# Kernel tuning notes

Measured on AMD Instinct MI355X. Metric: run time of the kernel, lower is better.

Reference implementation:

```python
import jax, jax.numpy as jnp
import numpy as np

B, S, D, H = 4, 2048, 1024, 16
DH = D // H  # head dim = 64


def setup_inputs() -> dict:
    key = jax.random.key(0)
    ks = jax.random.split(key, 7)
    q = jax.random.normal(ks[0], (B, S, D), dtype=jnp.float32)
    k = jax.random.normal(ks[1], (B, S, D), dtype=jnp.float32)
    v = jax.random.normal(ks[2], (B, S, D), dtype=jnp.float32)
    mask = jax.random.uniform(ks[3], (1, S, S), dtype=jnp.float32)
    sc = 1.0 / np.sqrt(D)
    Wq = jax.random.normal(ks[4], (D, D), dtype=jnp.float32) * sc
    Wk = jax.random.normal(ks[5], (D, D), dtype=jnp.float32) * sc
    Wv = jax.random.normal(ks[6], (D, D), dtype=jnp.float32) * sc
    return {"q": q, "k": k, "v": v, "mask": mask, "Wq": Wq, "Wk": Wk, "Wv": Wv}


def reference(q, k, v, mask, Wq, Wk, Wv):
    # Linear projections (no bias), then split hidden into H heads.
    # tf.concat(tf.split(x, H, axis=2), axis=0) == reshape to (B,S,H,DH);
    # the final split/concat restores channel order [head0, head1, ...],
    # i.e. a plain (B,S,H,DH)->(B,S,D) reshape.
    qh = (q @ Wq).reshape(B, S, H, DH)
    kh = (k @ Wk).reshape(B, S, H, DH)
    vh = (v @ Wv).reshape(B, S, H, DH)
    score = jnp.einsum("bqhd,bkhd->bhqk", qh, kh) / jnp.sqrt(
        jnp.asarray(DH, dtype=q.dtype))
    # multiplicative mask applied BEFORE softmax (broadcast (1,Sq,Sk))
    score = score * mask[:, None, :, :][0:1].squeeze(0) if False else score * mask  # mask (1,Sq,Sk) broadcasts over (B,H,Sq,Sk)
    attn = jax.nn.softmax(score, axis=-1)
    out = jnp.einsum("bhqk,bkhd->bqhd", attn, vh).reshape(B, S, D)
    return out
```

## Files before the change

### kernel.cpp

```cpp
#include <hip/hip_runtime.h>

#define B_  4
#define S_  2048
#define D_  1024
#define H_  16
#define DH_ 64

typedef __attribute__((ext_vector_type(8))) short bf16x8;
typedef __attribute__((ext_vector_type(4))) float f32x4;
typedef __attribute__((ext_vector_type(16))) float f32x16;
typedef __attribute__((ext_vector_type(4))) unsigned short u16x4;

__device__ __forceinline__ unsigned short f2bf(float f) {
  union { float f; unsigned int u; } x; x.f = f;
  unsigned int u = x.u;
  unsigned int r = (u + 0x7fffu + ((u >> 16) & 1u)) >> 16;
  return (unsigned short)r;
}

__device__ __forceinline__ int cvtpk(float lo, float hi) {
  unsigned r;
  asm("v_cvt_pk_bf16_f32 %0, %1, %2" : "=v"(r) : "v"(lo), "v"(hi));
  return (int)r;
}

__global__ __launch_bounds__(256) void wtrans_kernel(const float* __restrict__ W0,
                                                     const float* __restrict__ W1,
                                                     const float* __restrict__ W2,
                                                     unsigned short* __restrict__ Wt) {
  __shared__ float t[32][33];
  const int z = blockIdx.z;
  const float* W = (z == 0) ? W0 : ((z == 1) ? W1 : W2);
  unsigned short* O = Wt + (size_t)z * (D_ * D_);
  const int n0 = blockIdx.x * 32, k0 = blockIdx.y * 32;
  const int tx = threadIdx.x, ty = threadIdx.y;
#pragma unroll
  for (int i = 0; i < 4; i++) t[ty + i * 8][tx] = W[(size_t)(k0 + ty + i * 8) * D_ + n0 + tx];
  __syncthreads();
#pragma unroll
  for (int i = 0; i < 4; i++)
    O[(size_t)(n0 + ty + i * 8) * D_ + k0 + tx] = f2bf(t[tx][ty + i * 8]);
}

__global__ __launch_bounds__(256) void proj_kernel(const float* __restrict__ X0,
                                                   const float* __restrict__ X1,
                                                   const float* __restrict__ X2,
                                                   const unsigned short* __restrict__ Wt,
                                                   unsigned short* __restrict__ Y0) {
  __shared__ __align__(16) unsigned short smem[2 * 128 * 72];
  unsigned short* Alds = smem;
  unsigned short* Blds = smem + 128 * 72;
  const int z = blockIdx.z;
  const float* X = (z == 0) ? X0 : ((z == 1) ? X1 : X2);
  const unsigned short* Wz = Wt + (size_t)z * (D_ * D_);
  unsigned short* Y = Y0 + (size_t)z * ((size_t)B_ * S_ * D_);
  const float osc = (z == 0) ? 0.18033688f : 1.0f;

  const int tid = threadIdx.x;
  const int lane = tid & 63, w = tid >> 6;
  const int wr = w >> 1, wc = w & 1;
  const int l15 = lane & 15, lg = lane >> 4;
  const int r0 = blockIdx.y * 128, c0 = blockIdx.x * 128;

  f32x4 acc[4][4];
#pragma unroll
  for (int m = 0; m < 4; m++)
#pragma unroll
    for (int n = 0; n < 4; n++) acc[m][n] = (f32x4){0.f, 0.f, 0.f, 0.f};

  for (int kt = 0; kt < 16; ++kt) {
    __syncthreads();
    {
      const int rr = tid >> 4, cf = (tid & 15) * 4;
#pragma unroll
      for (int p = 0; p < 8; p++) {
        int row = rr + p * 16;
        float4 xv = *(const float4*)(X + (size_t)(r0 + row) * D_ + kt * 64 + cf);
        u16x4 bb = { f2bf(xv.x), f2bf(xv.y), f2bf(xv.z), f2bf(xv.w) };
        *(u16x4*)(&Alds[row * 72 + cf]) = bb;
      }
      const int rb = tid >> 3, cb = tid & 7;
#pragma unroll
      for (int p = 0; p < 4; p++) {
        int row = rb + p * 32;
        bf16x8 wv = *(const bf16x8*)(Wz + (size_t)(c0 + row) * D_ + kt * 64 + cb * 8);
        *(bf16x8*)(&Blds[row * 72 + cb * 8]) = wv;
      }
    }
    __syncthreads();

    bf16x8 af[4][2];
#pragma unroll
    for (int m = 0; m < 4; m++)
#pragma unroll
      for (int kc = 0; kc < 2; kc++)
        af[m][kc] = *(const bf16x8*)(&Alds[(wr * 64 + m * 16 + l15) * 72 + kc * 32 + lg * 8]);
#pragma unroll
    for (int n = 0; n < 4; n++) {
      bf16x8 bfr[2];
#pragma unroll
      for (int kc = 0; kc < 2; kc++)
        bfr[kc] = *(const bf16x8*)(&Blds[(wc * 64 + n * 16 + l15) * 72 + kc * 32 + lg * 8]);
#pragma unroll
      for (int m = 0; m < 4; m++)
#pragma unroll
        for (int kc = 0; kc < 2; kc++)
          acc[m][n] = __builtin_amdgcn_mfma_f32_16x16x32_bf16(af[m][kc], bfr[kc], acc[m][n], 0, 0, 0);
    }
  }

  if (z == 2) {
    __syncthreads();
#pragma unroll
    for (int m = 0; m < 4; m++)
#pragma unroll
      for (int n = 0; n < 4; n++)
#pragma unroll
        for (int r = 0; r < 4; r++) {
          int srow = wr * 64 + m * 16 + lg * 4 + r;
          int dcol = wc * 64 + n * 16 + l15;
          smem[dcol * 136 + srow] = f2bf(acc[m][n][r]);
        }
    __syncthreads();
    const int dl = tid >> 1, sh = (tid & 1) * 64;
    const int bb = r0 >> 11, s0 = r0 & 2047;
    const int hh = (c0 + dl) >> 6, dd = (c0 + dl) & 63;
    size_t gbase = ((size_t)(bb * H_ + hh) * DH_ + dd) * (size_t)S_ + s0 + sh;
#pragma unroll
    for (int j = 0; j < 8; j++)
      *(bf16x8*)(Y + gbase + j * 8) = *(const bf16x8*)(&smem[dl * 136 + sh + j * 8]);
  } else {
#pragma unroll
    for (int m = 0; m < 4; m++)
#pragma unroll
      for (int n = 0; n < 4; n++)
#pragma unroll
        for (int r = 0; r < 4; r++) {
          int row = r0 + wr * 64 + m * 16 + lg * 4 + r;
          int col = c0 + wc * 64 + n * 16 + l15;
          Y[(size_t)row * D_ + col] = f2bf(acc[m][n][r] * osc);
        }
  }
}

__global__ __launch_bounds__(256) void attn_kernel(
    const unsigned short* __restrict__ qh,
    const unsigned short* __restrict__ kh,
    const unsigned short* __restrict__ vt,
    const float* __restrict__ mask,
    float* __restrict__ out) {
  __shared__ __align__(16) unsigned short K_lds[2][64 * 72];
  __shared__ __align__(16) unsigned short V_lds[2][64 * 72];

  const int tid = threadIdx.x;
  const int lane = tid & 63, w = tid >> 6;
  const int l31 = lane & 31, hf = lane >> 5;
  const int q0 = blockIdx.x * 128;
  const int h = blockIdx.y, b = blockIdx.z;
  const size_t head = (size_t)b * S_ * D_ + h * DH_;
  const int qrow = q0 + w * 32 + l31;

  bf16x8 bq[4];
  {
    const unsigned short* qp = qh + head + (size_t)qrow * D_;
#pragma unroll
    for (int ds = 0; ds < 4; ds++) bq[ds] = *(const bf16x8*)(qp + ds * 16 + hf * 8);
  }

  const int rr = tid >> 3, cc = tid & 7;
  const unsigned short* kbase = kh + head + (size_t)rr * D_ + cc * 8;
  const unsigned short* vtb = vt + ((size_t)(b * H_ + h) * DH_ + rr) * (size_t)S_ + cc * 8;

  f32x16 o_acc[2];
#pragma unroll
  for (int dt = 0; dt < 2; dt++)
#pragma unroll
    for (int r = 0; r < 16; r++) o_acc[dt][r] = 0.f;
  float m_r = -INFINITY, l_r = 0.f;

  {
#pragma unroll
    for (int p = 0; p < 2; p++) {
      bf16x8 kreg = *(const bf16x8*)(kbase + (size_t)p * 32 * D_);
      bf16x8 vreg = *(const bf16x8*)(vtb + (size_t)p * 32 * S_);
      int row = rr + p * 32;
      *(bf16x8*)(&K_lds[0][row * 72 + cc * 8]) = kreg;
      int byt = (row * 144 + cc * 16) ^ (((row >> 3) & 7) << 4);
      *(bf16x8*)((char*)&V_lds[0][0] + byt) = vreg;
    }
    __syncthreads();
  }

  for (int kt = 0; kt < 32; kt++) {
    const int cur = kt & 1;
    const bool more = (kt + 1 < 32);

    const int ktn = more ? kt + 1 : kt;
    bf16x8 kreg2[2], vreg2[2];
#pragma unroll
    for (int p = 0; p < 2; p++) {
      kreg2[p] = *(const bf16x8*)(kbase + (size_t)ktn * 64 * D_ + (size_t)p * 32 * D_);
      vreg2[p] = *(const bf16x8*)(vtb + (size_t)ktn * 64 + (size_t)p * 32 * S_);
    }
    __builtin_amdgcn_sched_barrier(0);

    f32x16 sacc[2];
#pragma unroll
    for (int ct = 0; ct < 2; ct++)
#pragma unroll
      for (int r = 0; r < 16; r++) sacc[ct][r] = 0.f;
    __builtin_amdgcn_s_setprio(1);
#pragma unroll
    for (int ds = 0; ds < 4; ds++)
#pragma unroll
      for (int ct = 0; ct < 2; ct++) {
        bf16x8 ak = *(const bf16x8*)(&K_lds[cur][(ct * 32 + l31) * 72 + ds * 16 + hf * 8]);
        sacc[ct] = __builtin_amdgcn_mfma_f32_32x32x16_bf16(ak, bq[ds], sacc[ct], 0, 0, 0);
      }
    __builtin_amdgcn_s_setprio(0);

    const float* mrow = mask + (size_t)qrow * S_ + kt * 64 + hf * 4;
#pragma unroll
    for (int ct = 0; ct < 2; ct++)
#pragma unroll
      for (int rq = 0; rq < 4; rq++) {
        float4 mk = *(const float4*)(mrow + ct * 32 + rq * 8);
        sacc[ct][rq * 4 + 0] *= mk.x;
        sacc[ct][rq * 4 + 1] *= mk.y;
        sacc[ct][rq * 4 + 2] *= mk.z;
        sacc[ct][rq * 4 + 3] *= mk.w;
      }

    float red[16];
#pragma unroll
    for (int i = 0; i < 16; i++) red[i] = fmaxf(sacc[0][i], sacc[1][i]);
#pragma unroll
    for (int off = 8; off >= 1; off >>= 1)
#pragma unroll
      for (int i = 0; i < off; i++) red[i] = fmaxf(red[i], red[i + off]);
    float tm = fmaxf(red[0], __shfl_xor(red[0], 32));

    float mn;
    if (__any(tm > m_r + 8.0f)) {
      mn = fmaxf(m_r, tm);
      float alpha = exp2f(m_r - mn);
      m_r = mn;
      l_r *= alpha;
#pragma unroll
      for (int dt = 0; dt < 2; dt++)
#pragma unroll
        for (int r = 0; r < 16; r++) o_acc[dt][r] *= alpha;
    } else {
      mn = m_r;
    }

#pragma unroll
    for (int ct = 0; ct < 2; ct++)
#pragma unroll
      for (int r = 0; r < 16; r++) sacc[ct][r] = exp2f(sacc[ct][r] - mn);

    float sr[16];
#pragma unroll
    for (int i = 0; i < 16; i++) sr[i] = sacc[0][i] + sacc[1][i];
#pragma unroll
    for (int off = 8; off >= 1; off >>= 1)
#pragma unroll
      for (int i = 0; i < off; i++) sr[i] += sr[i + off];
    l_r += sr[0] + __shfl_xor(sr[0], 32);

    bf16x8 bfp[4];
#pragma unroll
    for (int s = 0; s < 4; s++) {
      const int ct = s >> 1, rb = (s & 1) * 8;
      int L1 = cvtpk(sacc[ct][rb + 0], sacc[ct][rb + 1]);
      int L2 = cvtpk(sacc[ct][rb + 2], sacc[ct][rb + 3]);
      int H1 = cvtpk(sacc[ct][rb + 4], sacc[ct][rb + 5]);
      int H2 = cvtpk(sacc[ct][rb + 6], sacc[ct][rb + 7]);
      int xL1 = __shfl_xor(L1, 32), xL2 = __shfl_xor(L2, 32);
      int xH1 = __shfl_xor(H1, 32), xH2 = __shfl_xor(H2, 32);
      union { int u[4]; bf16x8 v; } cv;
      cv.u[0] = hf ? xH1 : L1;
      cv.u[1] = hf ? xH2 : L2;
      cv.u[2] = hf ? H1 : xL1;
      cv.u[3] = hf ? H2 : xL2;
      bfp[s] = cv.v;
    }

    __builtin_amdgcn_s_setprio(1);
#pragma unroll
    for (int dt = 0; dt < 2; dt++) {
      const int d0 = dt * 32 + l31;
      const int bbase = d0 * 144;
      const int swz = ((d0 >> 3) & 7) << 4;
#pragma unroll
      for (int s = 0; s < 4; s++) {
        int byt = (bbase + (s * 16 + hf * 8) * 2) ^ swz;
        bf16x8 av = *(const bf16x8*)((const char*)&V_lds[cur][0] + byt);
        o_acc[dt] = __builtin_amdgcn_mfma_f32_32x32x16_bf16(av, bfp[s], o_acc[dt], 0, 0, 0);
      }
    }
    __builtin_amdgcn_s_setprio(0);

    if (more) {
#pragma unroll
      for (int p = 0; p < 2; p++) {
        int row = rr + p * 32;
        *(bf16x8*)(&K_lds[cur ^ 1][row * 72 + cc * 8]) = kreg2[p];
        int byt = (row * 144 + cc * 16) ^ (((row >> 3) & 7) << 4);
        *(bf16x8*)((char*)&V_lds[cur ^ 1][0] + byt) = vreg2[p];
      }
      __syncthreads();
    }
  }

  const float invl = 1.0f / l_r;
  float* op = out + (size_t)(b * S_ + qrow) * D_ + h * DH_;
#pragma unroll
  for (int dt = 0; dt < 2; dt++)
#pragma unroll
    for (int rq = 0; rq < 4; rq++) {
      float4 ov = { o_acc[dt][rq * 4 + 0] * invl, o_acc[dt][rq * 4 + 1] * invl,
                    o_acc[dt][rq * 4 + 2] * invl, o_acc[dt][rq * 4 + 3] * invl };
      *(float4*)(op + dt * 32 + rq * 8 + hf * 4) = ov;
    }
}

extern "C" void kernel_launch(void* const* d_in, const int* in_sizes, int n_in,
                              void* d_out, int out_size, void* d_ws, size_t ws_size,
                              hipStream_t stream) {
  const float* q = (const float*)d_in[0];
  const float* k = (const float*)d_in[1];
  const float* v = (const float*)d_in[2];
  const float* mask = (const float*)d_in[3];
  const float* Wq = (const float*)d_in[4];
  const float* Wk = (const float*)d_in[5];
  const float* Wv = (const float*)d_in[6];

  char* ws = (char*)d_ws;
  const size_t SZ_PROJ = (size_t)B_ * S_ * D_ * 2;
  unsigned short* qh = (unsigned short*)(ws);
  unsigned short* kh = (unsigned short*)(ws + SZ_PROJ);
  unsigned short* vhT = (unsigned short*)(ws + 2 * SZ_PROJ);
  unsigned short* Wt = (unsigned short*)(ws + 3 * SZ_PROJ);

  wtrans_kernel<<<dim3(D_ / 32, D_ / 32, 3), dim3(32, 8), 0, stream>>>(Wq, Wk, Wv, Wt);
  proj_kernel<<<dim3(D_ / 128, (B_ * S_) / 128, 3), 256, 0, stream>>>(q, k, v, Wt, qh);
  attn_kernel<<<dim3(S_ / 128, H_, B_), 256, 0, stream>>>(qh, kh, vhT, mask, (float*)d_out);
}
```

Before: 335.0 us.

## Load K/V fragments directly from global into registers, drop LDS staging

The attention kernel stops staging K and V tiles through double-buffered shared memory with a barrier per tile. Each wave now loads its own MFMA operand fragments for K and V straight from global memory into registers. The next K tile is prefetched right after the QK MFMAs, and the mask loads are hoisted to the top of the iteration. This removes LDS writes and reads and the per-tile __syncthreads. In exchange, each of the four waves re-reads the same K/V data from global memory or cache, and register pressure rises.

```diff
diff --git a/kernel.cpp b/kernel.cpp
--- a/kernel.cpp
+++ b/kernel.cpp
@@ -149,9 +149,6 @@
     const unsigned short* __restrict__ vt,
     const float* __restrict__ mask,
     float* __restrict__ out) {
-  __shared__ __align__(16) unsigned short K_lds[2][64 * 72];
-  __shared__ __align__(16) unsigned short V_lds[2][64 * 72];
-
   const int tid = threadIdx.x;
   const int lane = tid & 63, w = tid >> 6;
   const int l31 = lane & 31, hf = lane >> 5;
@@ -167,9 +164,12 @@
     for (int ds = 0; ds < 4; ds++) bq[ds] = *(const bf16x8*)(qp + ds * 16 + hf * 8);
   }
 
-  const int rr = tid >> 3, cc = tid & 7;
-  const unsigned short* kbase = kh + head + (size_t)rr * D_ + cc * 8;
-  const unsigned short* vtb = vt + ((size_t)(b * H_ + h) * DH_ + rr) * (size_t)S_ + cc * 8;
+  const unsigned short* kb0 = kh + head + (size_t)l31 * D_ + hf * 8;
+  const unsigned short* kb1 = kb0 + 32 * D_;
+  const unsigned short* vb0 = vt + ((size_t)(b * H_ + h) * DH_ + l31) * S_ + hf * 8;
+  const unsigned short* vb1 = vb0 + 32 * S_;
+  const float* mb0 = mask + (size_t)qrow * S_ + hf * 4;
+  const float* mb1 = mb0 + 32;
 
   f32x16 o_acc[2];
 #pragma unroll
@@ -178,30 +178,32 @@
     for (int r = 0; r < 16; r++) o_acc[dt][r] = 0.f;
   float m_r = -INFINITY, l_r = 0.f;
 
-  {
-#pragma unroll
-    for (int p = 0; p < 2; p++) {
-      bf16x8 kreg = *(const bf16x8*)(kbase + (size_t)p * 32 * D_);
-      bf16x8 vreg = *(const bf16x8*)(vtb + (size_t)p * 32 * S_);
-      int row = rr + p * 32;
-      *(bf16x8*)(&K_lds[0][row * 72 + cc * 8]) = kreg;
-      int byt = (row * 144 + cc * 16) ^ (((row >> 3) & 7) << 4);
-      *(bf16x8*)((char*)&V_lds[0][0] + byt) = vreg;
-    }
-    __syncthreads();
-  }
+  bf16x8 kfr[8];
+#pragma unroll
+  for (int ds = 0; ds < 4; ds++) {
+    kfr[0 * 4 + ds] = *(const bf16x8*)(kb0 + ds * 16);
+    kfr[1 * 4 + ds] = *(const bf16x8*)(kb1 + ds * 16);
+  }
+  kb0 += 64 * D_;
+  kb1 += 64 * D_;
 
   for (int kt = 0; kt < 32; kt++) {
-    const int cur = kt & 1;
-    const bool more = (kt + 1 < 32);
-
-    const int ktn = more ? kt + 1 : kt;
-    bf16x8 kreg2[2], vreg2[2];
-#pragma unroll
-    for (int p = 0; p < 2; p++) {
-      kreg2[p] = *(const bf16x8*)(kbase + (size_t)ktn * 64 * D_ + (size_t)p * 32 * D_);
-      vreg2[p] = *(const bf16x8*)(vtb + (size_t)ktn * 64 + (size_t)p * 32 * S_);
-    }
+    bf16x8 vfr[8];
+#pragma unroll
+    for (int s = 0; s < 4; s++) {
+      vfr[0 * 4 + s] = *(const bf16x8*)(vb0 + s * 16);
+      vfr[1 * 4 + s] = *(const bf16x8*)(vb1 + s * 16);
+    }
+    vb0 += 64;
+    vb1 += 64;
+    float4 mk[8];
+#pragma unroll
+    for (int rq = 0; rq < 4; rq++) {
+      mk[0 * 4 + rq] = *(const float4*)(mb0 + rq * 8);
+      mk[1 * 4 + rq] = *(const float4*)(mb1 + rq * 8);
+    }
+    mb0 += 64;
+    mb1 += 64;
     __builtin_amdgcn_sched_barrier(0);
 
     f32x16 sacc[2];
@@ -213,22 +215,28 @@
 #pragma unroll
     for (int ds = 0; ds < 4; ds++)
 #pragma unroll
-      for (int ct = 0; ct < 2; ct++) {
-        bf16x8 ak = *(const bf16x8*)(&K_lds[cur][(ct * 32 + l31) * 72 + ds * 16 + hf * 8]);
-        sacc[ct] = __builtin_amdgcn_mfma_f32_32x32x16_bf16(ak, bq[ds], sacc[ct], 0, 0, 0);
-      }
+      for (int ct = 0; ct < 2; ct++)
+        sacc[ct] = __builtin_amdgcn_mfma_f32_32x32x16_bf16(kfr[ct * 4 + ds], bq[ds], sacc[ct], 0, 0, 0);
     __builtin_amdgcn_s_setprio(0);
-
-    const float* mrow = mask + (size_t)qrow * S_ + kt * 64 + hf * 4;
+    __builtin_amdgcn_sched_barrier(0);
+
+#pragma unroll
+    for (int ds = 0; ds < 4; ds++) {
+      kfr[0 * 4 + ds] = *(const bf16x8*)(kb0 + ds * 16);
+      kfr[1 * 4 + ds] = *(const bf16x8*)(kb1 + ds * 16);
+    }
+    kb0 += 64 * D_;
+    kb1 += 64 * D_;
+    __builtin_amdgcn_sched_barrier(0);
+
 #pragma unroll
     for (int ct = 0; ct < 2; ct++)
 #pragma unroll
       for (int rq = 0; rq < 4; rq++) {
-        float4 mk = *(const float4*)(mrow + ct * 32 + rq * 8);
-        sacc[ct][rq * 4 + 0] *= mk.x;
-        sacc[ct][rq * 4 + 1] *= mk.y;
-        sacc[ct][rq * 4 + 2] *= mk.z;
-        sacc[ct][rq * 4 + 3] *= mk.w;
+        sacc[ct][rq * 4 + 0] *= mk[ct * 4 + rq].x;
+        sacc[ct][rq * 4 + 1] *= mk[ct * 4 + rq].y;
+        sacc[ct][rq * 4 + 2] *= mk[ct * 4 + rq].z;
+        sacc[ct][rq * 4 + 3] *= mk[ct * 4 + rq].w;
       }
 
     float red[16];
@@ -288,29 +296,11 @@
 
     __builtin_amdgcn_s_setprio(1);
 #pragma unroll
-    for (int dt = 0; dt < 2; dt++) {
-      const int d0 = dt * 32 + l31;
-      const int bbase = d0 * 144;
-      const int swz = ((d0 >> 3) & 7) << 4;
-#pragma unroll
-      for (int s = 0; s < 4; s++) {
-        int byt = (bbase + (s * 16 + hf * 8) * 2) ^ swz;
-        bf16x8 av = *(const bf16x8*)((const char*)&V_lds[cur][0] + byt);
-        o_acc[dt] = __builtin_amdgcn_mfma_f32_32x32x16_bf16(av, bfp[s], o_acc[dt], 0, 0, 0);
-      }
-    }
+    for (int dt = 0; dt < 2; dt++)
+#pragma unroll
+      for (int s = 0; s < 4; s++)
+        o_acc[dt] = __builtin_amdgcn_mfma_f32_32x32x16_bf16(vfr[dt * 4 + s], bfp[s], o_acc[dt], 0, 0, 0);
     __builtin_amdgcn_s_setprio(0);
-
-    if (more) {
-#pragma unroll
-      for (int p = 0; p < 2; p++) {
-        int row = rr + p * 32;
-        *(bf16x8*)(&K_lds[cur ^ 1][row * 72 + cc * 8]) = kreg2[p];
-        int byt = (row * 144 + cc * 16) ^ (((row >> 3) & 7) << 4);
-        *(bf16x8*)((char*)&V_lds[cur ^ 1][0] + byt) = vreg2[p];
-      }
-      __syncthreads();
-    }
   }
 
   const float invl = 1.0f / l_r;
```

After: 471.6 us. 1.41x slower.

## Software-pipeline attention loop with triple-buffered LDS and QK overlap

Applied to the files above, without the earlier changes.

Restructures the attention inner loop into a two-stage software pipeline. The QK^T MFMA for the next tile is issued while softmax and PV run on the current tile, and K/V go into a triple-buffered LDS ring with prefetch two tiles ahead. Mask loads are hoisted before the compute of each step. The aim is to hide the MFMA latency and the global load latency behind the softmax VALU work, at the cost of more registers and LDS, which may reduce occupancy.

```diff
diff --git a/kernel.cpp b/kernel.cpp
--- a/kernel.cpp
+++ b/kernel.cpp
@@ -149,8 +149,8 @@
     const unsigned short* __restrict__ vt,
     const float* __restrict__ mask,
     float* __restrict__ out) {
-  __shared__ __align__(16) unsigned short K_lds[2][64 * 72];
-  __shared__ __align__(16) unsigned short V_lds[2][64 * 72];
+  __shared__ __align__(16) unsigned short K_lds[3][64 * 72];
+  __shared__ __align__(16) unsigned short V_lds[3][64 * 72];
 
   const int tid = threadIdx.x;
   const int lane = tid & 63, w = tid >> 6;
@@ -170,6 +170,7 @@
   const int rr = tid >> 3, cc = tid & 7;
   const unsigned short* kbase = kh + head + (size_t)rr * D_ + cc * 8;
   const unsigned short* vtb = vt + ((size_t)(b * H_ + h) * DH_ + rr) * (size_t)S_ + cc * 8;
+  const float* mbase = mask + (size_t)qrow * S_ + hf * 4;
 
   f32x16 o_acc[2];
 #pragma unroll
@@ -178,68 +179,64 @@
     for (int r = 0; r < 16; r++) o_acc[dt][r] = 0.f;
   float m_r = -INFINITY, l_r = 0.f;
 
-  {
+  bf16x8 kpf[2], vpf[2];
+  float4 mk[8];
+  f32x16 qkA[2], qkB[2];
+
+  auto PREF = [&](int t) {
 #pragma unroll
     for (int p = 0; p < 2; p++) {
-      bf16x8 kreg = *(const bf16x8*)(kbase + (size_t)p * 32 * D_);
-      bf16x8 vreg = *(const bf16x8*)(vtb + (size_t)p * 32 * S_);
+      kpf[p] = *(const bf16x8*)(kbase + (size_t)t * 64 * D_ + (size_t)p * 32 * D_);
+      vpf[p] = *(const bf16x8*)(vtb + t * 64 + (size_t)p * 32 * S_);
+    }
+  };
+  auto STW = [&](int bf) {
+#pragma unroll
+    for (int p = 0; p < 2; p++) {
       int row = rr + p * 32;
-      *(bf16x8*)(&K_lds[0][row * 72 + cc * 8]) = kreg;
+      *(bf16x8*)(&K_lds[bf][row * 72 + cc * 8]) = kpf[p];
       int byt = (row * 144 + cc * 16) ^ (((row >> 3) & 7) << 4);
-      *(bf16x8*)((char*)&V_lds[0][0] + byt) = vreg;
-    }
-    __syncthreads();
-  }
-
-  for (int kt = 0; kt < 32; kt++) {
-    const int cur = kt & 1;
-    const bool more = (kt + 1 < 32);
-
-    const int ktn = more ? kt + 1 : kt;
-    bf16x8 kreg2[2], vreg2[2];
-#pragma unroll
-    for (int p = 0; p < 2; p++) {
-      kreg2[p] = *(const bf16x8*)(kbase + (size_t)ktn * 64 * D_ + (size_t)p * 32 * D_);
-      vreg2[p] = *(const bf16x8*)(vtb + (size_t)ktn * 64 + (size_t)p * 32 * S_);
-    }
-    __builtin_amdgcn_sched_barrier(0);
-
-    f32x16 sacc[2];
+      *(bf16x8*)((char*)&V_lds[bf][0] + byt) = vpf[p];
+    }
+  };
+  auto LDMASK = [&](int kt) {
+    const float* mrow = mbase + kt * 64;
 #pragma unroll
     for (int ct = 0; ct < 2; ct++)
 #pragma unroll
-      for (int r = 0; r < 16; r++) sacc[ct][r] = 0.f;
-    __builtin_amdgcn_s_setprio(1);
+      for (int rq = 0; rq < 4; rq++) mk[ct * 4 + rq] = *(const float4*)(mrow + ct * 32 + rq * 8);
+  };
+  auto QKT = [&](int bf, f32x16 (&qk)[2]) {
+#pragma unroll
+    for (int ct = 0; ct < 2; ct++)
+#pragma unroll
+      for (int r = 0; r < 16; r++) qk[ct][r] = 0.f;
 #pragma unroll
     for (int ds = 0; ds < 4; ds++)
 #pragma unroll
       for (int ct = 0; ct < 2; ct++) {
-        bf16x8 ak = *(const bf16x8*)(&K_lds[cur][(ct * 32 + l31) * 72 + ds * 16 + hf * 8]);
-        sacc[ct] = __builtin_amdgcn_mfma_f32_32x32x16_bf16(ak, bq[ds], sacc[ct], 0, 0, 0);
-      }
-    __builtin_amdgcn_s_setprio(0);
-
-    const float* mrow = mask + (size_t)qrow * S_ + kt * 64 + hf * 4;
+        bf16x8 ak = *(const bf16x8*)(&K_lds[bf][(ct * 32 + l31) * 72 + ds * 16 + hf * 8]);
+        qk[ct] = __builtin_amdgcn_mfma_f32_32x32x16_bf16(ak, bq[ds], qk[ct], 0, 0, 0);
+      }
+  };
+  auto SMPV = [&](f32x16 (&s)[2], int bv) {
 #pragma unroll
     for (int ct = 0; ct < 2; ct++)
 #pragma unroll
       for (int rq = 0; rq < 4; rq++) {
-        float4 mk = *(const float4*)(mrow + ct * 32 + rq * 8);
-        sacc[ct][rq * 4 + 0] *= mk.x;
-        sacc[ct][rq * 4 + 1] *= mk.y;
-        sacc[ct][rq * 4 + 2] *= mk.z;
-        sacc[ct][rq * 4 + 3] *= mk.w;
-      }
-
+        s[ct][rq * 4 + 0] *= mk[ct * 4 + rq].x;
+        s[ct][rq * 4 + 1] *= mk[ct * 4 + rq].y;
+        s[ct][rq * 4 + 2] *= mk[ct * 4 + rq].z;
+        s[ct][rq * 4 + 3] *= mk[ct * 4 + rq].w;
+      }
     float red[16];
 #pragma unroll
-    for (int i = 0; i < 16; i++) red[i] = fmaxf(sacc[0][i], sacc[1][i]);
+    for (int i = 0; i < 16; i++) red[i] = fmaxf(s[0][i], s[1][i]);
 #pragma unroll
     for (int off = 8; off >= 1; off >>= 1)
 #pragma unroll
       for (int i = 0; i < off; i++) red[i] = fmaxf(red[i], red[i + off]);
     float tm = fmaxf(red[0], __shfl_xor(red[0], 32));
-
     float mn;
     if (__any(tm > m_r + 8.0f)) {
       mn = fmaxf(m_r, tm);
@@ -253,29 +250,26 @@
     } else {
       mn = m_r;
     }
-
 #pragma unroll
     for (int ct = 0; ct < 2; ct++)
 #pragma unroll
-      for (int r = 0; r < 16; r++) sacc[ct][r] = exp2f(sacc[ct][r] - mn);
-
+      for (int r = 0; r < 16; r++) s[ct][r] = exp2f(s[ct][r] - mn);
     float sr[16];
 #pragma unroll
-    for (int i = 0; i < 16; i++) sr[i] = sacc[0][i] + sacc[1][i];
+    for (int i = 0; i < 16; i++) sr[i] = s[0][i] + s[1][i];
 #pragma unroll
     for (int off = 8; off >= 1; off >>= 1)
 #pragma unroll
       for (int i = 0; i < off; i++) sr[i] += sr[i + off];
     l_r += sr[0] + __shfl_xor(sr[0], 32);
-
     bf16x8 bfp[4];
 #pragma unroll
-    for (int s = 0; s < 4; s++) {
-      const int ct = s >> 1, rb = (s & 1) * 8;
-      int L1 = cvtpk(sacc[ct][rb + 0], sacc[ct][rb + 1]);
-      int L2 = cvtpk(sacc[ct][rb + 2], sacc[ct][rb + 3]);
-      int H1 = cvtpk(sacc[ct][rb + 4], sacc[ct][rb + 5]);
-      int H2 = cvtpk(sacc[ct][rb + 6], sacc[ct][rb + 7]);
+    for (int sx = 0; sx < 4; sx++) {
+      const int ct = sx >> 1, rb = (sx & 1) * 8;
+      int L1 = cvtpk(s[ct][rb + 0], s[ct][rb + 1]);
+      int L2 = cvtpk(s[ct][rb + 2], s[ct][rb + 3]);
+      int H1 = cvtpk(s[ct][rb + 4], s[ct][rb + 5]);
+      int H2 = cvtpk(s[ct][rb + 6], s[ct][rb + 7]);
       int xL1 = __shfl_xor(L1, 32), xL2 = __shfl_xor(L2, 32);
       int xH1 = __shfl_xor(H1, 32), xH2 = __shfl_xor(H2, 32);
       union { int u[4]; bf16x8 v; } cv;
@@ -283,9 +277,8 @@
       cv.u[1] = hf ? xH2 : L2;
       cv.u[2] = hf ? H1 : xL1;
       cv.u[3] = hf ? H2 : xL2;
-      bfp[s] = cv.v;
-    }
-
+      bfp[sx] = cv.v;
+    }
     __builtin_amdgcn_s_setprio(1);
 #pragma unroll
     for (int dt = 0; dt < 2; dt++) {
@@ -293,24 +286,47 @@
       const int bbase = d0 * 144;
       const int swz = ((d0 >> 3) & 7) << 4;
 #pragma unroll
-      for (int s = 0; s < 4; s++) {
-        int byt = (bbase + (s * 16 + hf * 8) * 2) ^ swz;
-        bf16x8 av = *(const bf16x8*)((const char*)&V_lds[cur][0] + byt);
-        o_acc[dt] = __builtin_amdgcn_mfma_f32_32x32x16_bf16(av, bfp[s], o_acc[dt], 0, 0, 0);
+      for (int sx = 0; sx < 4; sx++) {
+        int byt = (bbase + (sx * 16 + hf * 8) * 2) ^ swz;
+        bf16x8 av = *(const bf16x8*)((const char*)&V_lds[bv][0] + byt);
+        o_acc[dt] = __builtin_amdgcn_mfma_f32_32x32x16_bf16(av, bfp[sx], o_acc[dt], 0, 0, 0);
       }
     }
     __builtin_amdgcn_s_setprio(0);
-
-    if (more) {
-#pragma unroll
-      for (int p = 0; p < 2; p++) {
-        int row = rr + p * 32;
-        *(bf16x8*)(&K_lds[cur ^ 1][row * 72 + cc * 8]) = kreg2[p];
-        int byt = (row * 144 + cc * 16) ^ (((row >> 3) & 7) << 4);
-        *(bf16x8*)((char*)&V_lds[cur ^ 1][0] + byt) = vreg2[p];
-      }
-      __syncthreads();
-    }
+  };
+
+  PREF(0); STW(0);
+  PREF(1); STW(1);
+  __syncthreads();
+  QKT(0, qkA);
+
+  int bc = 0;
+  for (int it = 0; it < 15; ++it) {
+    const int t0 = 2 * it, t1 = t0 + 1;
+    const int b0 = bc, b1 = (b0 + 1 == 3) ? 0 : b0 + 1, b2 = (b1 + 1 == 3) ? 0 : b1 + 1;
+    PREF(t0 + 2);
+    LDMASK(t0);
+    __builtin_amdgcn_sched_barrier(0);
+    QKT(b1, qkB);
+    SMPV(qkA, b0);
+    STW(b2);
+    __syncthreads();
+    PREF(t1 + 2);
+    LDMASK(t1);
+    __builtin_amdgcn_sched_barrier(0);
+    QKT(b2, qkA);
+    SMPV(qkB, b1);
+    STW(b0);
+    __syncthreads();
+    bc = b2;
+  }
+  {
+    const int b0 = bc, b1 = (b0 + 1 == 3) ? 0 : b0 + 1;
+    LDMASK(30);
+    QKT(b1, qkB);
+    SMPV(qkA, b0);
+    LDMASK(31);
+    SMPV(qkB, b1);
   }
 
   const float invl = 1.0f / l_r;
```

Result: slower. 445.3 us (+32.9%).
